# Kernel optimization log

Measured on AMD Instinct MI355X. Metric: run time of the kernel, lower is better.

The kernel has to match this reference:

```python
import jax, jax.numpy as jnp
import numpy as np

B, N = 4, 128
INPUT_SIZE, Z_SIZE = 512, 256
D_TENSOR, N_HEADS, SEQ_LEN = 64, 8, 64
D = D_TENSOR * N_HEADS * SEQ_LEN  # 32768


def setup_inputs() -> dict:
    key = jax.random.key(0)
    ks = jax.random.split(key, 10)
    s = lambda fan_in: 1.0 / np.sqrt(fan_in)
    return {
        "x": jax.random.normal(ks[0], (B, N, INPUT_SIZE), dtype=jnp.float32),
        "z": jax.random.normal(ks[1], (B, N, Z_SIZE), dtype=jnp.float32),
        "Wq": jax.random.uniform(ks[2], (Z_SIZE, D), jnp.float32, -s(Z_SIZE), s(Z_SIZE)),
        "bq": jax.random.uniform(ks[3], (D,), jnp.float32, -s(Z_SIZE), s(Z_SIZE)),
        "Wk": jax.random.uniform(ks[4], (INPUT_SIZE, D), jnp.float32, -s(INPUT_SIZE), s(INPUT_SIZE)),
        "bk": jax.random.uniform(ks[5], (D,), jnp.float32, -s(INPUT_SIZE), s(INPUT_SIZE)),
        "Wv": jax.random.uniform(ks[6], (INPUT_SIZE, D), jnp.float32, -s(INPUT_SIZE), s(INPUT_SIZE)),
        "bv": jax.random.uniform(ks[7], (D,), jnp.float32, -s(INPUT_SIZE), s(INPUT_SIZE)),
        "Wo": jax.random.uniform(ks[8], (D, INPUT_SIZE), jnp.float32, -s(D), s(D)),
        "bo": jax.random.uniform(ks[9], (INPUT_SIZE,), jnp.float32, -s(D), s(D)),
    }


def reference(x, z, Wq, bq, Wk, bk, Wv, bv, Wo, bo):
    # Q, K, V: [B, N, heads, seq_len, d_tensor]
    Q = (z @ Wq + bq).reshape(B, N, N_HEADS, SEQ_LEN, D_TENSOR)
    K = (x @ Wk + bk).reshape(B, N, N_HEADS, SEQ_LEN, D_TENSOR)
    V = (x @ Wv + bv).reshape(B, N, N_HEADS, SEQ_LEN, D_TENSOR)
    scores = jnp.einsum("bnhqd,bnhkd->bnhqk", Q, K) / np.sqrt(D_TENSOR).astype(np.float32)
    attn = jax.nn.softmax(scores, axis=-1)
    out = jnp.einsum("bnhqk,bnhkd->bnhqd", attn, V).reshape(B, N, D)
    return out @ Wo + bo
```

## Files before the change

### kernel.cpp

```cpp
#include <hip/hip_runtime.h>
#include <stdint.h>


typedef __attribute__((ext_vector_type(8))) short short8;
typedef __attribute__((ext_vector_type(4))) float floatx4;

__device__ __forceinline__ unsigned short f2bf(float f) {
  union { float f; unsigned int u; } v; v.f = f;
  unsigned int u = v.u + 0x7FFFu + ((v.u >> 16) & 1u);
  return (unsigned short)(u >> 16);
}

__device__ __forceinline__ unsigned int cvt_pk_bf16(float lo, float hi) {
  unsigned int r;
  asm("v_cvt_pk_bf16_f32 %0, %1, %2" : "=v"(r) : "v"(lo), "v"(hi));
  return r;
}

#define MFMA16(a, b, c) __builtin_amdgcn_mfma_f32_16x16x32_bf16((a), (b), (c), 0, 0, 0)

#define STAGE_TILE(SRC, LD, LDSARR)                                            \
  do {                                                                         \
    _Pragma("unroll") for (int i_ = 0; i_ < 4; ++i_) {                         \
      int e_ = tid + (i_ << 8);                                                \
      int r_ = e_ >> 3;                                                        \
      int c_ = (e_ & 7) ^ (r_ & 7);                                            \
      __builtin_amdgcn_global_load_lds(                                        \
          (const __attribute__((address_space(1))) unsigned int*)((SRC) +      \
              (size_t)r_ * (LD) + (c_ << 3)),                                  \
          (__attribute__((address_space(3))) unsigned int*)(&(LDSARR)[e_ << 3]),\
          16, 0, 0);                                                           \
    }                                                                          \
  } while (0)

#define FRAG(LDSARR, ROW, KS)                                                  \
  (*(const short8*)(&(LDSARR)[(((ROW) << 6)) +                                 \
      ((((((KS) << 2) + quad)) ^ ((ROW) & 7)) << 3)]))

template <int LDW>
__device__ __forceinline__ void b_issue(const float* __restrict__ Wp,
                                        float* fB, int n, int octb) {
#pragma unroll
  for (int g = 0; g < 4; ++g) {
    const int oct = octb + 2 * g;
    const float* src = Wp + (size_t)(oct << 3) * LDW + n;
#pragma unroll
    for (int j = 0; j < 8; ++j) fB[g * 8 + j] = src[(size_t)j * LDW];
  }
}

__device__ __forceinline__ void b_write(unsigned short* Bs, const float* fB,
                                        int n, int octb) {
#pragma unroll
  for (int g = 0; g < 4; ++g) {
    const int oct = octb + 2 * g;
    uint4 p;
    p.x = cvt_pk_bf16(fB[g * 8 + 0], fB[g * 8 + 1]);
    p.y = cvt_pk_bf16(fB[g * 8 + 2], fB[g * 8 + 3]);
    p.z = cvt_pk_bf16(fB[g * 8 + 4], fB[g * 8 + 5]);
    p.w = cvt_pk_bf16(fB[g * 8 + 6], fB[g * 8 + 7]);
    *(uint4*)(&Bs[(n << 6) + ((oct ^ (n & 7)) << 3)]) = p;
  }
}

__global__ __launch_bounds__(256) void convert_xz(const float* __restrict__ x,
                                                  const float* __restrict__ z,
                                                  unsigned short* __restrict__ xb,
                                                  unsigned short* __restrict__ zb) {
  int idx = (blockIdx.x * 256 + threadIdx.x) * 8;
  const float* src;
  unsigned short* dst;
  if (idx < 262144) { src = x + idx; dst = xb + idx; }
  else              { src = z + (idx - 262144); dst = zb + (idx - 262144); }
  float4 f0 = *(const float4*)src;
  float4 f1 = *(const float4*)(src + 4);
  uint4 p;
  p.x = f2bf(f0.x) | ((unsigned)f2bf(f0.y) << 16);
  p.y = f2bf(f0.z) | ((unsigned)f2bf(f0.w) << 16);
  p.z = f2bf(f1.x) | ((unsigned)f2bf(f1.y) << 16);
  p.w = f2bf(f1.z) | ((unsigned)f2bf(f1.w) << 16);
  *(uint4*)dst = p;
}

__global__ __launch_bounds__(256, 3) void gemm_qkv(const unsigned short* __restrict__ xb,
                                                   const unsigned short* __restrict__ zb,
                                                   const float* __restrict__ Wq,
                                                   const float* __restrict__ Wk,
                                                   const float* __restrict__ Wv,
                                                   const float* __restrict__ bq,
                                                   const float* __restrict__ bk,
                                                   const float* __restrict__ bv,
                                                   unsigned short* __restrict__ Qb,
                                                   unsigned short* __restrict__ Kb,
                                                   unsigned short* __restrict__ Vb) {
  __shared__ __align__(16) unsigned short As[2][128 * 64];
  __shared__ __align__(16) unsigned short Bs[128 * 64];
  const int tid = threadIdx.x;
  const int zsel = blockIdx.z;
  const unsigned short* A;
  const float* W;
  const float* bias;
  unsigned short* C;
  int Ka;
  if (zsel == 0)      { A = zb; W = Wq; bias = bq; C = Qb; Ka = 256; }
  else if (zsel == 1) { A = xb; W = Wk; bias = bk; C = Kb; Ka = 512; }
  else                { A = xb; W = Wv; bias = bv; C = Vb; Ka = 512; }
  const int id = blockIdx.x;
  const int xcd = id & 7, bj = id >> 3;
  const int m0 = (bj & 3) << 7;
  const int n0 = ((xcd << 5) | (bj >> 2)) << 7;
  const int lane = tid & 63, wid = tid >> 6;
  const int quad = lane >> 4, l15 = lane & 15;
  const int wm = wid >> 1, wn = wid & 1;
  const int n = tid & 127;
  const int octb = __builtin_amdgcn_readfirstlane(tid >> 7);
  const int nsteps = Ka >> 6;

  float fB[32];
  floatx4 acc[4][4] = {};

  STAGE_TILE(A + (size_t)m0 * Ka, Ka, As[0]);
  __builtin_amdgcn_sched_barrier(0);
  b_issue<32768>(W + n0, fB, n, octb);
  __builtin_amdgcn_sched_barrier(0);

  for (int t = 0; t < nsteps; ++t) {
    const int cur = t & 1;
    b_write(Bs, fB, n, octb);
    asm volatile("s_waitcnt vmcnt(0) lgkmcnt(0)" ::: "memory");
    __builtin_amdgcn_s_barrier();
    __builtin_amdgcn_sched_barrier(0);
    if (t + 1 < nsteps) {
      STAGE_TILE(A + (size_t)m0 * Ka + ((t + 1) << 6), Ka, As[cur ^ 1]);
      __builtin_amdgcn_sched_barrier(0);
      b_issue<32768>(W + ((size_t)(t + 1) << 6) * 32768 + n0, fB, n, octb);
    }
    __builtin_amdgcn_sched_barrier(0);
#pragma unroll
    for (int ks = 0; ks < 2; ++ks) {
      short8 aF[4], bF[4];
#pragma unroll
      for (int mi = 0; mi < 4; ++mi) aF[mi] = FRAG(As[cur], wm * 64 + mi * 16 + l15, ks);
#pragma unroll
      for (int ni = 0; ni < 4; ++ni) bF[ni] = FRAG(Bs, wn * 64 + ni * 16 + l15, ks);
#pragma unroll
      for (int mi = 0; mi < 4; ++mi)
#pragma unroll
        for (int ni = 0; ni < 4; ++ni)
          acc[mi][ni] = MFMA16(aF[mi], bF[ni], acc[mi][ni]);
    }
    __builtin_amdgcn_s_barrier();
  }
#pragma unroll
  for (int ni = 0; ni < 4; ++ni) {
    int col = n0 + wn * 64 + ni * 16 + l15;
    float bv2 = bias[col];
#pragma unroll
    for (int mi = 0; mi < 4; ++mi) {
      int row = m0 + wm * 64 + mi * 16 + (quad << 2);
#pragma unroll
      for (int r = 0; r < 4; ++r)
        C[(size_t)(row + r) * 32768 + col] = f2bf(acc[mi][ni][r] + bv2);
    }
  }
}

__global__ __launch_bounds__(256) void attn64(const unsigned short* __restrict__ Qb,
                                              const unsigned short* __restrict__ Kb,
                                              const unsigned short* __restrict__ Vb,
                                              unsigned short* __restrict__ Ob) {
  __shared__ __align__(16) unsigned short Qs[64 * 72];
  __shared__ __align__(16) unsigned short Ks[64 * 72];
  __shared__ __align__(16) unsigned short VT[64 * 72];
  __shared__ __align__(16) unsigned short Ps[64 * 72];
  const int tid = threadIdx.x;
  const int bn = blockIdx.x >> 3, h = blockIdx.x & 7;
  const size_t base = (size_t)bn * 32768 + (size_t)h * 4096;
  const unsigned short* q = Qb + base;
  const unsigned short* k = Kb + base;
  const unsigned short* v = Vb + base;
#pragma unroll
  for (int i = 0; i < 2; ++i) {
    int e = tid + (i << 8);
    int r = e >> 3, dblk = e & 7;
    *(uint4*)(&Qs[r * 72 + dblk * 8]) = *(const uint4*)(q + r * 64 + dblk * 8);
    *(uint4*)(&Ks[r * 72 + dblk * 8]) = *(const uint4*)(k + r * 64 + dblk * 8);
    uint4 vv = *(const uint4*)(v + r * 64 + dblk * 8);
    const unsigned short* pv = (const unsigned short*)&vv;
#pragma unroll
    for (int j = 0; j < 8; ++j)
      VT[(dblk * 8 + j) * 72 + r] = pv[j];
  }
  __syncthreads();
  const int lane = tid & 63, wid = tid >> 6;
  const int quad = lane >> 4, l15 = lane & 15;
  const int qs = wid << 4;
  short8 aq0 = *(const short8*)(&Qs[(qs + l15) * 72 + quad * 8]);
  short8 aq1 = *(const short8*)(&Qs[(qs + l15) * 72 + 32 + quad * 8]);
  floatx4 s[4] = {};
#pragma unroll
  for (int ni = 0; ni < 4; ++ni) {
    short8 b0 = *(const short8*)(&Ks[(ni * 16 + l15) * 72 + quad * 8]);
    short8 b1 = *(const short8*)(&Ks[(ni * 16 + l15) * 72 + 32 + quad * 8]);
    s[ni] = MFMA16(aq0, b0, s[ni]);
    s[ni] = MFMA16(aq1, b1, s[ni]);
  }
#pragma unroll
  for (int r = 0; r < 4; ++r) {
    float e0 = s[0][r] * 0.125f, e1 = s[1][r] * 0.125f;
    float e2 = s[2][r] * 0.125f, e3 = s[3][r] * 0.125f;
    float m = fmaxf(fmaxf(e0, e1), fmaxf(e2, e3));
    m = fmaxf(m, __shfl_xor(m, 1));
    m = fmaxf(m, __shfl_xor(m, 2));
    m = fmaxf(m, __shfl_xor(m, 4));
    m = fmaxf(m, __shfl_xor(m, 8));
    float x0 = __expf(e0 - m), x1 = __expf(e1 - m);
    float x2 = __expf(e2 - m), x3 = __expf(e3 - m);
    float t = x0 + x1 + x2 + x3;
    t += __shfl_xor(t, 1); t += __shfl_xor(t, 2);
    t += __shfl_xor(t, 4); t += __shfl_xor(t, 8);
    float inv = __builtin_amdgcn_rcpf(t);
    int row = qs + (quad << 2) + r;
    Ps[row * 72 +      l15] = f2bf(x0 * inv);
    Ps[row * 72 + 16 + l15] = f2bf(x1 * inv);
    Ps[row * 72 + 32 + l15] = f2bf(x2 * inv);
    Ps[row * 72 + 48 + l15] = f2bf(x3 * inv);
  }
  __syncthreads();
  short8 ap0 = *(const short8*)(&Ps[(qs + l15) * 72 + quad * 8]);
  short8 ap1 = *(const short8*)(&Ps[(qs + l15) * 72 + 32 + quad * 8]);
  floatx4 o[4] = {};
#pragma unroll
  for (int ni = 0; ni < 4; ++ni) {
    short8 b0 = *(const short8*)(&VT[(ni * 16 + l15) * 72 + quad * 8]);
    short8 b1 = *(const short8*)(&VT[(ni * 16 + l15) * 72 + 32 + quad * 8]);
    o[ni] = MFMA16(ap0, b0, o[ni]);
    o[ni] = MFMA16(ap1, b1, o[ni]);
  }
  unsigned short* outp = Ob + base;
#pragma unroll
  for (int ni = 0; ni < 4; ++ni)
#pragma unroll
    for (int r = 0; r < 4; ++r)
      outp[(qs + (quad << 2) + r) * 64 + ni * 16 + l15] = f2bf(o[ni][r]);
}

__global__ __launch_bounds__(256, 3) void gemm_out(const unsigned short* __restrict__ A,
                                                   const float* __restrict__ Wo,
                                                   float* __restrict__ Cp) {
  __shared__ __align__(16) unsigned short As[2][128 * 64];
  __shared__ __align__(16) unsigned short Bs[128 * 64];
  const int tid = threadIdx.x;
  const int id = blockIdx.x;
  const int xcd = id & 7, bj = id >> 3;
  const int m0 = (bj & 3) << 7;
  const int q = bj >> 2;
  const int n0 = (q & 3) << 7;
  const int ks = (xcd << 2) | (q >> 2);
  const int kbase = ks << 10;
  const int lane = tid & 63, wid = tid >> 6;
  const int quad = lane >> 4, l15 = lane & 15;
  const int wm = wid >> 1, wn = wid & 1;
  const int n = tid & 127;
  const int octb = __builtin_amdgcn_readfirstlane(tid >> 7);
  const int nsteps = 16;

  float fB[32];
  floatx4 acc[4][4] = {};

  STAGE_TILE(A + (size_t)m0 * 32768 + kbase, 32768, As[0]);
  __builtin_amdgcn_sched_barrier(0);
  b_issue<512>(Wo + (size_t)kbase * 512 + n0, fB, n, octb);
  __builtin_amdgcn_sched_barrier(0);

  for (int t = 0; t < nsteps; ++t) {
    const int cur = t & 1;
    b_write(Bs, fB, n, octb);
    asm volatile("s_waitcnt vmcnt(0) lgkmcnt(0)" ::: "memory");
    __builtin_amdgcn_s_barrier();
    __builtin_amdgcn_sched_barrier(0);
    if (t + 1 < nsteps) {
      STAGE_TILE(A + (size_t)m0 * 32768 + kbase + ((t + 1) << 6), 32768, As[cur ^ 1]);
      __builtin_amdgcn_sched_barrier(0);
      b_issue<512>(Wo + (size_t)(kbase + ((t + 1) << 6)) * 512 + n0, fB, n, octb);
    }
    __builtin_amdgcn_sched_barrier(0);
#pragma unroll
    for (int kss = 0; kss < 2; ++kss) {
      short8 aF[4], bF[4];
#pragma unroll
      for (int mi = 0; mi < 4; ++mi) aF[mi] = FRAG(As[cur], wm * 64 + mi * 16 + l15, kss);
#pragma unroll
      for (int ni = 0; ni < 4; ++ni) bF[ni] = FRAG(Bs, wn * 64 + ni * 16 + l15, kss);
#pragma unroll
      for (int mi = 0; mi < 4; ++mi)
#pragma unroll
        for (int ni = 0; ni < 4; ++ni)
          acc[mi][ni] = MFMA16(aF[mi], bF[ni], acc[mi][ni]);
    }
    __builtin_amdgcn_s_barrier();
  }
  float* outp = Cp + (size_t)ks * 262144;
#pragma unroll
  for (int ni = 0; ni < 4; ++ni) {
    int col = n0 + wn * 64 + ni * 16 + l15;
#pragma unroll
    for (int mi = 0; mi < 4; ++mi) {
      int row = m0 + wm * 64 + mi * 16 + (quad << 2);
#pragma unroll
      for (int r = 0; r < 4; ++r)
        outp[(size_t)(row + r) * 512 + col] = acc[mi][ni][r];
    }
  }
}

__global__ __launch_bounds__(256) void reduce_out(const float* __restrict__ Cp,
                                                  const float* __restrict__ bias,
                                                  float* __restrict__ C) {
  int idx = blockIdx.x * 256 + threadIdx.x;
  float s = bias[idx & 511];
#pragma unroll
  for (int k = 0; k < 32; ++k) s += Cp[(size_t)k * 262144 + idx];
  C[idx] = s;
}

extern "C" void kernel_launch(void* const* d_in, const int* in_sizes, int n_in,
                              void* d_out, int out_size, void* d_ws, size_t ws_size,
                              hipStream_t stream) {
  const float* x  = (const float*)d_in[0];
  const float* z  = (const float*)d_in[1];
  const float* Wq = (const float*)d_in[2];
  const float* bq = (const float*)d_in[3];
  const float* Wk = (const float*)d_in[4];
  const float* bk = (const float*)d_in[5];
  const float* Wv = (const float*)d_in[6];
  const float* bv = (const float*)d_in[7];
  const float* Wo = (const float*)d_in[8];
  const float* bo = (const float*)d_in[9];
  float* out = (float*)d_out;
  char* ws = (char*)d_ws;

  unsigned short* Qb = (unsigned short*)(ws + 0);
  unsigned short* Kb = (unsigned short*)(ws + 33554432);
  unsigned short* Vb = (unsigned short*)(ws + 67108864);
  unsigned short* Ob = (unsigned short*)(ws + 100663296);
  unsigned short* xb = (unsigned short*)(ws + 134217728);
  unsigned short* zb = (unsigned short*)(ws + 134742016);
  float*          Cp = (float*)(ws + 135266304);

  convert_xz<<<dim3(192), 256, 0, stream>>>(x, z, xb, zb);

  gemm_qkv<<<dim3(1024, 1, 3), 256, 0, stream>>>(xb, zb, Wq, Wk, Wv,
                                                 bq, bk, bv, Qb, Kb, Vb);

  attn64<<<dim3(4096), 256, 0, stream>>>(Qb, Kb, Vb, Ob);

  gemm_out<<<dim3(512), 256, 0, stream>>>(Ob, Wo, Cp);

  reduce_out<<<dim3(1024), 256, 0, stream>>>(Cp, bo, out);
}
```

Before: 334.1 us.

## Double-buffer fp32 weight tiles in registers and vectorize weight loads

Result: slower. 584.3 us (+74.9%).

```diff
diff --git a/kernel.cpp b/kernel.cpp
--- a/kernel.cpp
+++ b/kernel.cpp
@@ -38,28 +38,25 @@
       ((((((KS) << 2) + quad)) ^ ((ROW) & 7)) << 3)]))
 
 template <int LDW>
-__device__ __forceinline__ void b_issue(const float* __restrict__ Wp,
-                                        float* fB, int n, int octb) {
-#pragma unroll
-  for (int g = 0; g < 4; ++g) {
-    const int oct = octb + 2 * g;
-    const float* src = Wp + (size_t)(oct << 3) * LDW + n;
-#pragma unroll
-    for (int j = 0; j < 8; ++j) fB[g * 8 + j] = src[(size_t)j * LDW];
-  }
-}
-
-__device__ __forceinline__ void b_write(unsigned short* Bs, const float* fB,
-                                        int n, int octb) {
-#pragma unroll
-  for (int g = 0; g < 4; ++g) {
-    const int oct = octb + 2 * g;
+__device__ __forceinline__ void b_issue8(const float* __restrict__ Wp,
+                                         floatx4* f4, int g, int q) {
+  const float* src = Wp + (size_t)(g << 3) * LDW + (q << 2);
+#pragma unroll
+  for (int j = 0; j < 8; ++j)
+    f4[j] = *(const floatx4*)(src + (size_t)j * LDW);
+}
+
+__device__ __forceinline__ void b_write8(unsigned short* Bs, const floatx4* f4,
+                                         int g, int q) {
+#pragma unroll
+  for (int i = 0; i < 4; ++i) {
+    const int n = (q << 2) + i;
     uint4 p;
-    p.x = cvt_pk_bf16(fB[g * 8 + 0], fB[g * 8 + 1]);
-    p.y = cvt_pk_bf16(fB[g * 8 + 2], fB[g * 8 + 3]);
-    p.z = cvt_pk_bf16(fB[g * 8 + 4], fB[g * 8 + 5]);
-    p.w = cvt_pk_bf16(fB[g * 8 + 6], fB[g * 8 + 7]);
-    *(uint4*)(&Bs[(n << 6) + ((oct ^ (n & 7)) << 3)]) = p;
+    p.x = cvt_pk_bf16(f4[0][i], f4[1][i]);
+    p.y = cvt_pk_bf16(f4[2][i], f4[3][i]);
+    p.z = cvt_pk_bf16(f4[4][i], f4[5][i]);
+    p.w = cvt_pk_bf16(f4[6][i], f4[7][i]);
+    *(uint4*)(&Bs[(n << 6) + ((g ^ (n & 7)) << 3)]) = p;
   }
 }
 
@@ -112,29 +109,34 @@
   const int lane = tid & 63, wid = tid >> 6;
   const int quad = lane >> 4, l15 = lane & 15;
   const int wm = wid >> 1, wn = wid & 1;
-  const int n = tid & 127;
-  const int octb = __builtin_amdgcn_readfirstlane(tid >> 7);
+  const int g = tid >> 5, q = tid & 31;
   const int nsteps = Ka >> 6;
 
-  float fB[32];
+  floatx4 fA[8], fBr[8];
   floatx4 acc[4][4] = {};
 
+  b_issue8<32768>(W + n0, fA, g, q);
+  __builtin_amdgcn_sched_barrier(0);
   STAGE_TILE(A + (size_t)m0 * Ka, Ka, As[0]);
   __builtin_amdgcn_sched_barrier(0);
-  b_issue<32768>(W + n0, fB, n, octb);
+  b_issue8<32768>(W + (size_t)64 * 32768 + n0, fBr, g, q);
   __builtin_amdgcn_sched_barrier(0);
 
   for (int t = 0; t < nsteps; ++t) {
     const int cur = t & 1;
-    b_write(Bs, fB, n, octb);
-    asm volatile("s_waitcnt vmcnt(0) lgkmcnt(0)" ::: "memory");
+    floatx4* Fc = (t & 1) ? fBr : fA;
+    if (t < nsteps - 1) { asm volatile("s_waitcnt vmcnt(8)" ::: "memory"); }
+    else                { asm volatile("s_waitcnt vmcnt(0)" ::: "memory"); }
+    __builtin_amdgcn_sched_barrier(0);
+    b_write8(Bs, Fc, g, q);
+    asm volatile("s_waitcnt lgkmcnt(0)" ::: "memory");
     __builtin_amdgcn_s_barrier();
     __builtin_amdgcn_sched_barrier(0);
-    if (t + 1 < nsteps) {
+    if (t + 1 < nsteps)
       STAGE_TILE(A + (size_t)m0 * Ka + ((t + 1) << 6), Ka, As[cur ^ 1]);
-      __builtin_amdgcn_sched_barrier(0);
-      b_issue<32768>(W + ((size_t)(t + 1) << 6) * 32768 + n0, fB, n, octb);
-    }
+    __builtin_amdgcn_sched_barrier(0);
+    if (t + 2 < nsteps)
+      b_issue8<32768>(W + ((size_t)(t + 2) << 6) * 32768 + n0, Fc, g, q);
     __builtin_amdgcn_sched_barrier(0);
 #pragma unroll
     for (int ks = 0; ks < 2; ++ks) {
@@ -254,36 +256,41 @@
   const int id = blockIdx.x;
   const int xcd = id & 7, bj = id >> 3;
   const int m0 = (bj & 3) << 7;
-  const int q = bj >> 2;
-  const int n0 = (q & 3) << 7;
-  const int ks = (xcd << 2) | (q >> 2);
+  const int qq = bj >> 2;
+  const int n0 = (qq & 3) << 7;
+  const int ks = (xcd << 2) | (qq >> 2);
   const int kbase = ks << 10;
   const int lane = tid & 63, wid = tid >> 6;
   const int quad = lane >> 4, l15 = lane & 15;
   const int wm = wid >> 1, wn = wid & 1;
-  const int n = tid & 127;
-  const int octb = __builtin_amdgcn_readfirstlane(tid >> 7);
+  const int g = tid >> 5, q = tid & 31;
   const int nsteps = 16;
 
-  float fB[32];
+  floatx4 fA[8], fBr[8];
   floatx4 acc[4][4] = {};
 
+  b_issue8<512>(Wo + (size_t)kbase * 512 + n0, fA, g, q);
+  __builtin_amdgcn_sched_barrier(0);
   STAGE_TILE(A + (size_t)m0 * 32768 + kbase, 32768, As[0]);
   __builtin_amdgcn_sched_barrier(0);
-  b_issue<512>(Wo + (size_t)kbase * 512 + n0, fB, n, octb);
+  b_issue8<512>(Wo + (size_t)(kbase + 64) * 512 + n0, fBr, g, q);
   __builtin_amdgcn_sched_barrier(0);
 
   for (int t = 0; t < nsteps; ++t) {
     const int cur = t & 1;
-    b_write(Bs, fB, n, octb);
-    asm volatile("s_waitcnt vmcnt(0) lgkmcnt(0)" ::: "memory");
+    floatx4* Fc = (t & 1) ? fBr : fA;
+    if (t < nsteps - 1) { asm volatile("s_waitcnt vmcnt(8)" ::: "memory"); }
+    else                { asm volatile("s_waitcnt vmcnt(0)" ::: "memory"); }
+    __builtin_amdgcn_sched_barrier(0);
+    b_write8(Bs, Fc, g, q);
+    asm volatile("s_waitcnt lgkmcnt(0)" ::: "memory");
     __builtin_amdgcn_s_barrier();
     __builtin_amdgcn_sched_barrier(0);
-    if (t + 1 < nsteps) {
+    if (t + 1 < nsteps)
       STAGE_TILE(A + (size_t)m0 * 32768 + kbase + ((t + 1) << 6), 32768, As[cur ^ 1]);
-      __builtin_amdgcn_sched_barrier(0);
-      b_issue<512>(Wo + (size_t)(kbase + ((t + 1) << 6)) * 512 + n0, fB, n, octb);
-    }
+    __builtin_amdgcn_sched_barrier(0);
+    if (t + 2 < nsteps)
+      b_issue8<512>(Wo + (size_t)(kbase + ((t + 2) << 6)) * 512 + n0, Fc, g, q);
     __builtin_amdgcn_sched_barrier(0);
 #pragma unroll
     for (int kss = 0; kss < 2; ++kss) {
```
